# Performance work log

Hardware: AMD Instinct MI355X
Metric: run time of the kernel (lower is better)

The kernel has to match this reference:

```python
import jax, jax.numpy as jnp
import numpy as np


def setup_inputs() -> dict:
    key = jax.random.key(0)
    ks = jax.random.split(key, 7)
    B, U, I, D, K = 16384, 100000, 1000000, 64, 16
    F = 2 * D
    stdv = 1.0 / np.sqrt(D)
    return {
        "user": jax.random.randint(ks[0], (B,), 0, U),
        "item": jax.random.randint(ks[1], (B,), 0, I),
        "user_emb": jax.random.normal(ks[2], (U, D), jnp.float32) * stdv,
        "item_emb": jax.random.normal(ks[3], (I, D), jnp.float32) * stdv,
        "w1": jax.random.normal(ks[4], (F, 1), jnp.float32) * stdv,
        "b1": jax.random.normal(ks[5], (1,), jnp.float32) * stdv,
        "v": jax.random.normal(ks[6], (F, K), jnp.float32) * stdv,
    }


def reference(user, item, user_emb, item_emb, w1, b1, v):
    # x: [B, 2*dim]
    x = jnp.concatenate([user_emb[user], item_emb[item]], axis=-1)
    # first-order term: Linear(feat_dim, 1) then squeeze -> [B]
    lin = (x @ w1 + b1)[:, 0]
    # second-order: sum_{i<j} x_i x_j (v v^T)_{ij}
    # == 0.5 * sum_k ((x @ v)_k^2 - (x^2 @ v^2)_k)  (FM identity)
    xv = x @ v                      # [B, k]
    x2v2 = (x * x) @ (v * v)        # [B, k]
    pair = 0.5 * jnp.sum(xv * xv - x2v2, axis=-1)
    return lin + pair
```

## Files before the change

### kernel.cpp

```cpp
#include <hip/hip_runtime.h>

#define DIMS 64
#define KF 16
#define F 128
#define ROWS 4
#define ROWS_PER_BLOCK 16

template<int CTRL>
__device__ __forceinline__ float dppmv(float x) {
    return __builtin_bit_cast(float,
        __builtin_amdgcn_update_dpp(0, __builtin_bit_cast(int, x), CTRL, 0xF, 0xF, true));
}
template<int PAT>
__device__ __forceinline__ float swzf(float x) {
    return __builtin_bit_cast(float,
        __builtin_amdgcn_ds_swizzle(__builtin_bit_cast(int, x), PAT));
}

#define DPP_XOR1  0xB1
#define DPP_XOR2  0x4E
#define DPP_XOR8  0x128
#define SWZ_XOR4  0x101F
#define SWZ_XOR16 0x401F

__device__ __forceinline__ float sum_xor16(float x) {
#if __has_builtin(__builtin_amdgcn_permlane16_swap)
    auto r = __builtin_amdgcn_permlane16_swap(__builtin_bit_cast(int, x),
                                              __builtin_bit_cast(int, x), false, false);
    return __builtin_bit_cast(float, (int)r[0]) + __builtin_bit_cast(float, (int)r[1]);
#else
    return x + swzf<SWZ_XOR16>(x);
#endif
}
__device__ __forceinline__ float sum_xor32(float x) {
#if __has_builtin(__builtin_amdgcn_permlane32_swap)
    auto r = __builtin_amdgcn_permlane32_swap(__builtin_bit_cast(int, x),
                                              __builtin_bit_cast(int, x), false, false);
    return __builtin_bit_cast(float, (int)r[0]) + __builtin_bit_cast(float, (int)r[1]);
#else
    return x + __shfl_xor(x, 32, 64);
#endif
}

__global__ __launch_bounds__(256, 4) void fm_fwd_kernel(
    const int* __restrict__ user,
    const int* __restrict__ item,
    const float* __restrict__ user_emb,
    const float* __restrict__ item_emb,
    const float* __restrict__ w1,
    const float* __restrict__ b1,
    const float* __restrict__ v,
    float* __restrict__ out,
    int B)
{
    __shared__ float vsT[KF * F];

    const int tid  = threadIdx.x;
    const int lane = tid & 63;
    const int wv   = tid >> 6;
    const int q    = lane & 31;
    const int half = lane >> 5;

    const float4* vg = (const float4*)v;
    const float4 p0 = vg[tid * 2 + 0];
    const float4 p1 = vg[tid * 2 + 1];

    const int base = __builtin_amdgcn_readfirstlane(
        (int)blockIdx.x * ROWS_PER_BLOCK + wv * ROWS);
    int ui[ROWS], ti[ROWS];
    if ((int)(blockIdx.x + 1) * ROWS_PER_BLOCK <= B) {
        const int4 uu = *(const int4*)(user + base);
        const int4 tt = *(const int4*)(item + base);
        ui[0] = uu.x; ui[1] = uu.y; ui[2] = uu.z; ui[3] = uu.w;
        ti[0] = tt.x; ti[1] = tt.y; ti[2] = tt.z; ti[3] = tt.w;
    } else {
        #pragma unroll
        for (int r = 0; r < ROWS; ++r) {
            const int i = min(base + r, B - 1);
            ui[r] = user[i];
            ti[r] = item[i];
        }
    }

    float2 x[ROWS];
    #pragma unroll
    for (int r = 0; r < ROWS; ++r) {
        const float* src = half ? (item_emb + (size_t)ti[r] * DIMS)
                                : (user_emb + (size_t)ui[r] * DIMS);
        x[r] = *(const float2*)(src + 2 * q);
    }

    const float2 w2 = *(const float2*)(w1 + half * DIMS + 2 * q);
    const float bias = b1[0];

    {
        const int f  = tid >> 1;
        const int k0 = (tid & 1) * 8;
        vsT[(k0+0)*F + f] = p0.x;  vsT[(k0+1)*F + f] = p0.y;
        vsT[(k0+2)*F + f] = p0.z;  vsT[(k0+3)*F + f] = p0.w;
        vsT[(k0+4)*F + f] = p1.x;  vsT[(k0+5)*F + f] = p1.y;
        vsT[(k0+6)*F + f] = p1.z;  vsT[(k0+7)*F + f] = p1.w;
    }
    asm volatile("s_waitcnt lgkmcnt(0)" ::: "memory");
    __builtin_amdgcn_s_barrier();

    const float2* vs2 = ((const float2*)vsT) + lane;
    float s0[KF], s1[KF], s2[KF], s3[KF];
    float A0 = 0.f, A1 = 0.f;
    #pragma unroll
    for (int k = 0; k < KF; ++k) {
        const float2 vv = vs2[k * 64];
        A0 += vv.x * vv.x;
        A1 += vv.y * vv.y;
        s0[k] = x[0].x * vv.x + x[0].y * vv.y;
        s1[k] = x[1].x * vv.x + x[1].y * vv.y;
        s2[k] = x[2].x * vv.x + x[2].y * vv.y;
        s3[k] = x[3].x * vv.x + x[3].y * vv.y;
    }
    float c[ROWS];
    #pragma unroll
    for (int r = 0; r < ROWS; ++r)
        c[r] = x[r].x * w2.x + x[r].y * w2.y
             - 0.5f * (x[r].x * x[r].x * A0 + x[r].y * x[r].y * A1);

    #define HALVE2(SA, SB, MV, M, N) { \
        const bool hi = (lane & (M)) != 0; \
        _Pragma("unroll") \
        for (int i = 0; i < (N); ++i) { \
            float kA = hi ? SA[(N)+i] : SA[i]; float dA = hi ? SA[i] : SA[(N)+i]; \
            float kB = hi ? SB[(N)+i] : SB[i]; float dB = hi ? SB[i] : SB[(N)+i]; \
            SA[i] = kA + MV(dA); \
            SB[i] = kB + MV(dB); \
        } }
    #define REDUCE_PAIR(SA, SB, CA, CB) { \
        HALVE2(SA, SB, dppmv<DPP_XOR1>, 1, 8) \
        HALVE2(SA, SB, dppmv<DPP_XOR2>, 2, 4) \
        HALVE2(SA, SB, dppmv<DPP_XOR8>, 8, 2) \
        HALVE2(SA, SB, swzf<SWZ_XOR4>,  4, 1) \
        float svA = sum_xor32(sum_xor16(SA[0])); \
        float svB = sum_xor32(sum_xor16(SB[0])); \
        CA += 0.125f * svA * svA; \
        CB += 0.125f * svB * svB; \
    }
    REDUCE_PAIR(s0, s1, c[0], c[1])
    REDUCE_PAIR(s2, s3, c[2], c[3])
    #undef REDUCE_PAIR
    #undef HALVE2

    float r0, r1;
    {
        const bool hi = (lane & 1) != 0;
        float k0 = hi ? c[2] : c[0], d0 = hi ? c[0] : c[2];
        float k1 = hi ? c[3] : c[1], d1 = hi ? c[1] : c[3];
        r0 = k0 + dppmv<DPP_XOR1>(d0);
        r1 = k1 + dppmv<DPP_XOR1>(d1);
    }
    float rr;
    {
        const bool hi = (lane & 2) != 0;
        float kk = hi ? r1 : r0, dd = hi ? r0 : r1;
        rr = kk + dppmv<DPP_XOR2>(dd);
    }
    rr += swzf<SWZ_XOR4>(rr);
    rr += dppmv<DPP_XOR8>(rr);
    rr = sum_xor16(rr);
    rr = sum_xor32(rr);

    if (lane < ROWS) {
        const int row = ((lane & 1) << 1) | ((lane >> 1) & 1);
        if (base + row < B)
            out[base + row] = bias + rr;
    }
}

extern "C" void kernel_launch(void* const* d_in, const int* in_sizes, int n_in,
                              void* d_out, int out_size, void* d_ws, size_t ws_size,
                              hipStream_t stream) {
    const int*   user     = (const int*)  d_in[0];
    const int*   item     = (const int*)  d_in[1];
    const float* user_emb = (const float*)d_in[2];
    const float* item_emb = (const float*)d_in[3];
    const float* w1       = (const float*)d_in[4];
    const float* b1       = (const float*)d_in[5];
    const float* v        = (const float*)d_in[6];
    float* out = (float*)d_out;

    const int B = in_sizes[0];
    const int blocks = (B + ROWS_PER_BLOCK - 1) / ROWS_PER_BLOCK;
    fm_fwd_kernel<<<blocks, 256, 0, stream>>>(user, item, user_emb, item_emb,
                                              w1, b1, v, out, B);
}
```

Baseline: 9.735 us.

## Process eight rows per wavefront in two groups of four

Doubles the rows handled by each wavefront from four to eight, giving thirty-two rows per block and half as many blocks. The LDS transpose of v and the block setup are amortised over more rows, and eight independent gathers can be in flight per wave. The compute and reduce path runs twice per wave over groups of four rows. In exchange, register pressure rises and the grid has fewer blocks to spread across the GPU.

```diff
diff --git a/kernel.cpp b/kernel.cpp
--- a/kernel.cpp
+++ b/kernel.cpp
@@ -3,8 +3,8 @@
 #define DIMS 64
 #define KF 16
 #define F 128
-#define ROWS 4
-#define ROWS_PER_BLOCK 16
+#define ROWS 8
+#define ROWS_PER_BLOCK 32
 
 template<int CTRL>
 __device__ __forceinline__ float dppmv(float x) {
@@ -69,10 +69,14 @@
         (int)blockIdx.x * ROWS_PER_BLOCK + wv * ROWS);
     int ui[ROWS], ti[ROWS];
     if ((int)(blockIdx.x + 1) * ROWS_PER_BLOCK <= B) {
-        const int4 uu = *(const int4*)(user + base);
-        const int4 tt = *(const int4*)(item + base);
-        ui[0] = uu.x; ui[1] = uu.y; ui[2] = uu.z; ui[3] = uu.w;
-        ti[0] = tt.x; ti[1] = tt.y; ti[2] = tt.z; ti[3] = tt.w;
+        const int4 u0 = *(const int4*)(user + base);
+        const int4 u1 = *(const int4*)(user + base + 4);
+        const int4 t0 = *(const int4*)(item + base);
+        const int4 t1 = *(const int4*)(item + base + 4);
+        ui[0]=u0.x; ui[1]=u0.y; ui[2]=u0.z; ui[3]=u0.w;
+        ui[4]=u1.x; ui[5]=u1.y; ui[6]=u1.z; ui[7]=u1.w;
+        ti[0]=t0.x; ti[1]=t0.y; ti[2]=t0.z; ti[3]=t0.w;
+        ti[4]=t1.x; ti[5]=t1.y; ti[6]=t1.z; ti[7]=t1.w;
     } else {
         #pragma unroll
         for (int r = 0; r < ROWS; ++r) {
@@ -105,23 +109,9 @@
     __builtin_amdgcn_s_barrier();
 
     const float2* vs2 = ((const float2*)vsT) + lane;
-    float s0[KF], s1[KF], s2[KF], s3[KF];
+
+    float rrA, rrB;
     float A0 = 0.f, A1 = 0.f;
-    #pragma unroll
-    for (int k = 0; k < KF; ++k) {
-        const float2 vv = vs2[k * 64];
-        A0 += vv.x * vv.x;
-        A1 += vv.y * vv.y;
-        s0[k] = x[0].x * vv.x + x[0].y * vv.y;
-        s1[k] = x[1].x * vv.x + x[1].y * vv.y;
-        s2[k] = x[2].x * vv.x + x[2].y * vv.y;
-        s3[k] = x[3].x * vv.x + x[3].y * vv.y;
-    }
-    float c[ROWS];
-    #pragma unroll
-    for (int r = 0; r < ROWS; ++r)
-        c[r] = x[r].x * w2.x + x[r].y * w2.y
-             - 0.5f * (x[r].x * x[r].x * A0 + x[r].y * x[r].y * A1);
 
     #define HALVE2(SA, SB, MV, M, N) { \
         const bool hi = (lane & (M)) != 0; \
@@ -142,34 +132,61 @@
         CA += 0.125f * svA * svA; \
         CB += 0.125f * svB * svB; \
     }
-    REDUCE_PAIR(s0, s1, c[0], c[1])
-    REDUCE_PAIR(s2, s3, c[2], c[3])
+
+    #pragma unroll
+    for (int g = 0; g < 2; ++g) {
+        const int o = g * 4;
+        float s0[KF], s1[KF], s2[KF], s3[KF];
+        #pragma unroll
+        for (int k = 0; k < KF; ++k) {
+            const float2 vv = vs2[k * 64];
+            if (g == 0) {
+                A0 += vv.x * vv.x;
+                A1 += vv.y * vv.y;
+            }
+            s0[k] = x[o+0].x * vv.x + x[o+0].y * vv.y;
+            s1[k] = x[o+1].x * vv.x + x[o+1].y * vv.y;
+            s2[k] = x[o+2].x * vv.x + x[o+2].y * vv.y;
+            s3[k] = x[o+3].x * vv.x + x[o+3].y * vv.y;
+        }
+        float c[4];
+        #pragma unroll
+        for (int r = 0; r < 4; ++r)
+            c[r] = x[o+r].x * w2.x + x[o+r].y * w2.y
+                 - 0.5f * (x[o+r].x * x[o+r].x * A0 + x[o+r].y * x[o+r].y * A1);
+
+        REDUCE_PAIR(s0, s1, c[0], c[1])
+        REDUCE_PAIR(s2, s3, c[2], c[3])
+
+        float r0, r1;
+        {
+            const bool hi = (lane & 1) != 0;
+            float k0 = hi ? c[2] : c[0], d0 = hi ? c[0] : c[2];
+            float k1 = hi ? c[3] : c[1], d1 = hi ? c[1] : c[3];
+            r0 = k0 + dppmv<DPP_XOR1>(d0);
+            r1 = k1 + dppmv<DPP_XOR1>(d1);
+        }
+        float rr;
+        {
+            const bool hi = (lane & 2) != 0;
+            float kk = hi ? r1 : r0, dd = hi ? r0 : r1;
+            rr = kk + dppmv<DPP_XOR2>(dd);
+        }
+        rr += swzf<SWZ_XOR4>(rr);
+        rr += dppmv<DPP_XOR8>(rr);
+        rr = sum_xor16(rr);
+        rr = sum_xor32(rr);
+        if (g == 0) rrA = rr; else rrB = rr;
+    }
     #undef REDUCE_PAIR
     #undef HALVE2
 
-    float r0, r1;
-    {
-        const bool hi = (lane & 1) != 0;
-        float k0 = hi ? c[2] : c[0], d0 = hi ? c[0] : c[2];
-        float k1 = hi ? c[3] : c[1], d1 = hi ? c[1] : c[3];
-        r0 = k0 + dppmv<DPP_XOR1>(d0);
-        r1 = k1 + dppmv<DPP_XOR1>(d1);
-    }
-    float rr;
-    {
-        const bool hi = (lane & 2) != 0;
-        float kk = hi ? r1 : r0, dd = hi ? r0 : r1;
-        rr = kk + dppmv<DPP_XOR2>(dd);
-    }
-    rr += swzf<SWZ_XOR4>(rr);
-    rr += dppmv<DPP_XOR8>(rr);
-    rr = sum_xor16(rr);
-    rr = sum_xor32(rr);
-
-    if (lane < ROWS) {
-        const int row = ((lane & 1) << 1) | ((lane >> 1) & 1);
-        if (base + row < B)
-            out[base + row] = bias + rr;
+    if (lane < 8) {
+        const int rloc = ((lane & 1) << 1) | ((lane >> 1) & 1);
+        const int row  = base + (lane >> 2) * 4 + rloc;
+        const float val = (lane < 4) ? rrA : rrB;
+        if (row < B)
+            out[row] = bias + val;
     }
 }
 
```

Result: slower. 11.50 us (+18.1%).
